# Kernel tuning notes

Hardware: AMD Instinct MI355X
Metric: run time of the kernel (lower is better)

The kernel has to match this reference:

```python
import jax, jax.numpy as jnp
import numpy as np

VOCAB = 32000
EMB = 512
HEADS = 8
HEAD_DIM = EMB // HEADS
MLP = 2048
LAYERS = 6
KERNEL_EPS = 1e-3  # performer generalized-attention kernel_epsilon
LN_EPS = 1e-6


def sinusoidal_pos_emb(seq_len, dim):
    pos = np.arange(seq_len)[:, None].astype(np.float32)
    div = np.exp(np.arange(0, dim, 2).astype(np.float32) * (-np.log(10000.0) / dim))
    pe = np.zeros((seq_len, dim), dtype=np.float32)
    pe[:, 0::2] = np.sin(pos * div)
    pe[:, 1::2] = np.cos(pos * div)
    return jnp.asarray(pe)


def setup_inputs() -> dict:
    key = jax.random.key(0)
    ks = jax.random.split(key, 16)
    B, S = 4, 4096
    s_emb = 1.0 / np.sqrt(EMB)
    s_head = 1.0 / np.sqrt(HEAD_DIM)
    s_mlp = 1.0 / np.sqrt(MLP)
    return {
        'tokens': jax.random.randint(ks[0], (B, S), 0, VOCAB),
        'embed': jax.random.normal(ks[1], (VOCAB, EMB), jnp.float32) * s_emb,
        'Wq': jax.random.normal(ks[2], (LAYERS, EMB, HEADS, HEAD_DIM), jnp.float32) * s_emb,
        'Wk': jax.random.normal(ks[3], (LAYERS, EMB, HEADS, HEAD_DIM), jnp.float32) * s_emb,
        'Wv': jax.random.normal(ks[4], (LAYERS, EMB, HEADS, HEAD_DIM), jnp.float32) * s_emb,
        'Wo': jax.random.normal(ks[5], (LAYERS, HEADS, HEAD_DIM, EMB), jnp.float32) * s_head,
        'ln1_s': jnp.ones((LAYERS, EMB), jnp.float32),
        'ln1_b': jnp.zeros((LAYERS, EMB), jnp.float32),
        'W1': jax.random.normal(ks[6], (LAYERS, EMB, MLP), jnp.float32) * s_emb,
        'b1': jnp.zeros((LAYERS, MLP), jnp.float32),
        'W2': jax.random.normal(ks[7], (LAYERS, MLP, EMB), jnp.float32) * s_mlp,
        'b2': jnp.zeros((LAYERS, EMB), jnp.float32),
        'ln2_s': jnp.ones((LAYERS, EMB), jnp.float32),
        'ln2_b': jnp.zeros((LAYERS, EMB), jnp.float32),
        'lnf_s': jnp.ones((EMB,), jnp.float32),
        'lnf_b': jnp.zeros((EMB,), jnp.float32),
    }


def layer_norm(x, s, b):
    mu = jnp.mean(x, axis=-1, keepdims=True)
    var = jnp.mean(jnp.square(x - mu), axis=-1, keepdims=True)
    return (x - mu) * jax.lax.rsqrt(var + LN_EPS) * s + b


def favor_generalized_attention(x, Wq, Wk, Wv, Wo):
    # Performer generalized attention, deterministic ReLU feature map,
    # renormalized (bidirectional): O(S * m * d) linear attention.
    q = jnp.einsum('bsd,dhf->bshf', x, Wq)
    k = jnp.einsum('bsd,dhf->bshf', x, Wk)
    v = jnp.einsum('bsd,dhf->bshf', x, Wv)
    pq = jax.nn.relu(q) + KERNEL_EPS  # phi(q): [B,S,H,F]
    pk = jax.nn.relu(k) + KERNEL_EPS  # phi(k)
    kv = jnp.einsum('bshf,bshe->bhfe', pk, v)          # [B,H,F,E]
    num = jnp.einsum('bshf,bhfe->bshe', pq, kv)        # numerator
    den = jnp.einsum('bshf,bhf->bsh', pq, pk.sum(axis=1))  # renormalizer
    attn = num / den[..., None]
    return jnp.einsum('bshe,hed->bsd', attn, Wo)


def reference(tokens, embed, Wq, Wk, Wv, Wo, ln1_s, ln1_b, W1, b1, W2, b2,
              ln2_s, ln2_b, lnf_s, lnf_b):
    B, S = tokens.shape
    x = embed[tokens] + sinusoidal_pos_emb(S, EMB)[None, :, :]
    for l in range(LAYERS):
        h = layer_norm(x, ln1_s[l], ln1_b[l])
        x = x + favor_generalized_attention(h, Wq[l], Wk[l], Wv[l], Wo[l])
        h = layer_norm(x, ln2_s[l], ln2_b[l])
        h = jax.nn.gelu(h @ W1[l] + b1[l]) @ W2[l] + b2[l]
        x = x + h
    return layer_norm(x, lnf_s, lnf_b)
```

## Files before the change

### kernel.cpp

```cpp
#include <hip/hip_runtime.h>

typedef float f32x4 __attribute__((ext_vector_type(4)));
typedef __bf16 bf16x8 __attribute__((ext_vector_type(8)));

#define NROWS 16384
#define SEQ   4096
#define EMBD  512
#define MLPD  2048

__device__ inline float gelu_tanh(float x) {
    float t = 0.7978845608028654f * (x + 0.044715f * x * x * x);
    float e = __expf(2.f * t);
    float th = 1.f - 2.f / (1.f + e);
    return 0.5f * x * (1.f + th);
}

#define GLOAD16(gp, lp)                                                        \
    __builtin_amdgcn_global_load_lds(                                          \
        (const __attribute__((address_space(1))) void*)(gp),                   \
        (__attribute__((address_space(3))) void*)(lp), 16, 0, 0)

__global__ void pos_kernel(float* __restrict__ pos) {
    int i = blockIdx.x * 256 + threadIdx.x;
    int s = i >> 8, j = i & 255;
    float div = __expf((float)j * (-2.f * 9.210340371976184f / 512.f));
    float a = (float)s * div;
    pos[(size_t)s * 512 + 2 * j]     = sinf(a);
    pos[(size_t)s * 512 + 2 * j + 1] = cosf(a);
}

__global__ void embed_kernel(const int* __restrict__ tokens,
                             const float* __restrict__ embed,
                             const float* __restrict__ pos,
                             float* __restrict__ x) {
    int row = blockIdx.x;
    int t = threadIdx.x;
    int s = row & (SEQ - 1);
    int tok = tokens[row];
    f32x4 e = *(const f32x4*)(embed + (size_t)tok * 512 + t * 4);
    f32x4 p = *(const f32x4*)(pos + (size_t)s * 512 + t * 4);
    e += p;
    *(f32x4*)(x + (size_t)row * 512 + t * 4) = e;
}

__global__ void transpose_bf16(const float* __restrict__ in, __bf16* __restrict__ out,
                               int K, int N, size_t in_lstride, size_t out_lstride) {
    __shared__ float tile[32][33];
    in  += (size_t)blockIdx.z * in_lstride;
    out += (size_t)blockIdx.z * out_lstride;
    int n0 = blockIdx.x * 32, k0 = blockIdx.y * 32;
    int tx = threadIdx.x, ty = threadIdx.y;
    #pragma unroll
    for (int i = 0; i < 32; i += 8)
        tile[ty + i][tx] = in[(size_t)(k0 + ty + i) * N + n0 + tx];
    __syncthreads();
    #pragma unroll
    for (int i = 0; i < 32; i += 8)
        out[(size_t)(n0 + ty + i) * K + k0 + tx] = (__bf16)tile[tx][ty + i];
}

template<int OUTBF>
__global__ __launch_bounds__(256) void ln_kernel(
    const float* __restrict__ x, const float* __restrict__ gamma,
    const float* __restrict__ beta, __bf16* __restrict__ outb,
    float* __restrict__ outf) {
    int lane = threadIdx.x & 63;
    size_t row = (size_t)blockIdx.x * 4 + (threadIdx.x >> 6);
    const float* xr = x + row * 512 + lane * 8;
    f32x4 v0 = *(const f32x4*)xr;
    f32x4 v1 = *(const f32x4*)(xr + 4);
    float sum = (v0[0] + v0[1]) + (v0[2] + v0[3]) + (v1[0] + v1[1]) + (v1[2] + v1[3]);
    #pragma unroll
    for (int off = 32; off; off >>= 1) sum += __shfl_xor(sum, off);
    float mu = sum * (1.f / 512.f);
    float vs = 0.f;
    #pragma unroll
    for (int j = 0; j < 4; j++) {
        float d0 = v0[j] - mu; vs += d0 * d0;
        float d1 = v1[j] - mu; vs += d1 * d1;
    }
    #pragma unroll
    for (int off = 32; off; off >>= 1) vs += __shfl_xor(vs, off);
    float inv = rsqrtf(vs * (1.f / 512.f) + 1e-6f);
    const float* gp = gamma + lane * 8;
    const float* bp = beta + lane * 8;
    f32x4 g0 = *(const f32x4*)gp, g1 = *(const f32x4*)(gp + 4);
    f32x4 bb0 = *(const f32x4*)bp, bb1 = *(const f32x4*)(bp + 4);
    float o[8];
    #pragma unroll
    for (int j = 0; j < 4; j++) {
        o[j]     = (v0[j] - mu) * inv * g0[j] + bb0[j];
        o[4 + j] = (v1[j] - mu) * inv * g1[j] + bb1[j];
    }
    if (OUTBF) {
        bf16x8 ov;
        #pragma unroll
        for (int j = 0; j < 8; j++) ov[j] = (__bf16)o[j];
        *(bf16x8*)(outb + row * 512 + lane * 8) = ov;
    } else {
        f32x4 o0 = {o[0], o[1], o[2], o[3]};
        f32x4 o1 = {o[4], o[5], o[6], o[7]};
        *(f32x4*)(outf + row * 512 + lane * 8) = o0;
        *(f32x4*)(outf + row * 512 + lane * 8 + 4) = o1;
    }
}

template<int EPI, int K>
__global__ __launch_bounds__(256, 4) void gemm_bt(
    const __bf16* __restrict__ A, const __bf16* __restrict__ BT,
    float* __restrict__ Cf, __bf16* __restrict__ Cb,
    const float* __restrict__ bias, int N, int nbn) {
    constexpr int NT = K / 32;
    __shared__ __align__(16) __bf16 Abuf[2][128 * 32];
    __shared__ __align__(16) __bf16 Bbuf[2][128 * 32];
    const int t = threadIdx.x;
    const int lane = t & 63;
    const int wave = t >> 6;
    const int wr = wave >> 1, wc = wave & 1;
    const int nblk = gridDim.x;
    const int q = nblk >> 3, r = nblk & 7;
    const int xcd = blockIdx.x & 7, loc = blockIdx.x >> 3;
    const int swz = (xcd < r ? xcd * (q + 1) : r * (q + 1) + (xcd - r) * q) + loc;
    const int m0 = (swz / nbn) * 128, n0 = (swz % nbn) * 128;
    const int fr = lane & 15, fc = lane >> 4;

    const __bf16* Aps[2];
    const __bf16* Bps[2];
    int lslot[2];
    #pragma unroll
    for (int j = 0; j < 2; j++) {
        int slot = t + 256 * j;
        int row = slot >> 2, cp = slot & 3;
        int sc = cp ^ ((row >> 1) & 3);
        Aps[j] = A  + (size_t)(m0 + row) * K + sc * 8;
        Bps[j] = BT + (size_t)(n0 + row) * K + sc * 8;
        lslot[j] = slot * 8;
    }

    f32x4 acc[4][4];
    #pragma unroll
    for (int m = 0; m < 4; m++)
        #pragma unroll
        for (int n = 0; n < 4; n++)
            acc[m][n] = (f32x4){0.f, 0.f, 0.f, 0.f};

    auto stage = [&](int koff, __bf16* Ad, __bf16* Bd) {
        #pragma unroll
        for (int j = 0; j < 2; j++) {
            GLOAD16(Aps[j] + koff, Ad + lslot[j]);
            GLOAD16(Bps[j] + koff, Bd + lslot[j]);
        }
    };

    int cur = 0;
    stage(0, Abuf[0], Bbuf[0]);

    for (int s = 0; s < NT; s++) {
        __bf16* Ac = Abuf[cur];     __bf16* Bc = Bbuf[cur];
        if (s + 1 < NT) {
            stage((s + 1) * 32, Abuf[cur ^ 1], Bbuf[cur ^ 1]);
            asm volatile("s_waitcnt vmcnt(4)" ::: "memory");
        } else {
            asm volatile("s_waitcnt vmcnt(0)" ::: "memory");
        }
        __builtin_amdgcn_s_barrier();

        bf16x8 af[4], bfr[4];
        #pragma unroll
        for (int m = 0; m < 4; m++) {
            int ra = wr * 64 + m * 16 + fr;
            int rb = wc * 64 + m * 16 + fr;
            af[m]  = *(const bf16x8*)(Ac + ra * 32 + ((fc ^ ((ra >> 1) & 3)) << 3));
            bfr[m] = *(const bf16x8*)(Bc + rb * 32 + ((fc ^ ((rb >> 1) & 3)) << 3));
        }
        __builtin_amdgcn_s_setprio(1);
        #pragma unroll
        for (int m = 0; m < 4; m++)
            #pragma unroll
            for (int n = 0; n < 4; n++)
                acc[m][n] = __builtin_amdgcn_mfma_f32_16x16x32_bf16(af[m], bfr[n], acc[m][n], 0, 0, 0);
        __builtin_amdgcn_s_setprio(0);
        __builtin_amdgcn_s_barrier();
        cur ^= 1;
    }

    const int cr = (lane >> 4) * 4;
    const int cc = lane & 15;
    #pragma unroll
    for (int m = 0; m < 4; m++) {
        #pragma unroll
        for (int n = 0; n < 4; n++) {
            #pragma unroll
            for (int r2 = 0; r2 < 4; r2++) {
                int grow = m0 + wr * 64 + m * 16 + cr + r2;
                int gcol = n0 + wc * 64 + n * 16 + cc;
                size_t idx = (size_t)grow * N + gcol;
                float val = acc[m][n][r2];
                if (EPI == 1) {
                    if (gcol < 1024) val = fmaxf(val, 0.f) + 1e-3f;
                    Cb[idx] = (__bf16)val;
                } else if (EPI == 2) {
                    Cf[idx] += val;
                } else if (EPI == 3) {
                    val += bias[gcol];
                    Cb[idx] = (__bf16)gelu_tanh(val);
                } else if (EPI == 4) {
                    Cf[idx] += val + bias[gcol];
                } else {
                    Cf[idx] = val;
                }
            }
        }
    }
}

__global__ __launch_bounds__(256) void kv_partial(const __bf16* __restrict__ qkvb,
                                                  float* __restrict__ part) {
    int bh = blockIdx.x;
    int chunk = blockIdx.y;
    int b = bh >> 3, hh = bh & 7;
    int t = threadIdx.x;
    int f = t & 63, eg = t >> 6;
    size_t base = ((size_t)b * SEQ + (size_t)chunk * 64) * 1536;
    const __bf16* kcol = qkvb + base + 512 + hh * 64 + f;
    const __bf16* vrow = qkvb + base + 1024 + hh * 64 + eg * 16;
    float psum = 0.f;
    f32x4 a0 = {0.f,0.f,0.f,0.f}, a1 = a0, a2 = a0, a3 = a0;
    for (int s = 0; s < 64; s++) {
        size_t o = (size_t)s * 1536;
        float pk = (float)kcol[o];
        psum += pk;
        bf16x8 w0 = *(const bf16x8*)(vrow + o);
        bf16x8 w1 = *(const bf16x8*)(vrow + o + 8);
        #pragma unroll
        for (int j = 0; j < 4; j++) {
            a0[j] += (float)w0[j]     * pk;
            a1[j] += (float)w0[4 + j] * pk;
            a2[j] += (float)w1[j]     * pk;
            a3[j] += (float)w1[4 + j] * pk;
        }
    }
    float* dst = part + ((size_t)chunk * 32 + bh) * 4160 + (size_t)f * 65 + eg * 16;
    #pragma unroll
    for (int j = 0; j < 4; j++) { dst[j] = a0[j]; dst[4+j] = a1[j]; dst[8+j] = a2[j]; dst[12+j] = a3[j]; }
    if (eg == 0) dst[64] = psum;
}

__global__ void kv_reduce(const float* __restrict__ part, float* __restrict__ kvfin) {
    int i = blockIdx.x * 256 + threadIdx.x;
    if (i >= 32 * 4160) return;
    float s = 0.f;
    #pragma unroll 8
    for (int c = 0; c < 64; c++) s += part[(size_t)c * (32 * 4160) + i];
    kvfin[i] = s;
}

__global__ __launch_bounds__(256) void num_attn(const __bf16* __restrict__ qkvb,
                                                const float* __restrict__ kvfin,
                                                __bf16* __restrict__ attn) {
    __shared__ float kvs[64][68];
    __shared__ float ps[64];
    int bh = blockIdx.x, chunk = blockIdx.y;
    int b = bh >> 3, hh = bh & 7;
    const float* src = kvfin + (size_t)bh * 4160;
    for (int i = threadIdx.x; i < 4160; i += 256) {
        int f = i / 65, e = i - f * 65;
        if (e < 64) kvs[f][e] = src[i]; else ps[f] = src[i];
    }
    __syncthreads();
    int t = threadIdx.x;
    int r = t >> 1, e0 = (t & 1) * 32;
    size_t row = (size_t)b * SEQ + (size_t)chunk * 128 + r;
    const __bf16* pqr = qkvb + row * 1536 + hh * 64;
    float pq[64];
    #pragma unroll
    for (int j = 0; j < 8; j++) {
        bf16x8 v = *(const bf16x8*)(pqr + 8 * j);
        #pragma unroll
        for (int k = 0; k < 8; k++) pq[8 * j + k] = (float)v[k];
    }
    float den = 0.f;
    #pragma unroll
    for (int f = 0; f < 64; f++) den += pq[f] * ps[f];
    f32x4 acc[8];
    #pragma unroll
    for (int j = 0; j < 8; j++) acc[j] = (f32x4){0.f,0.f,0.f,0.f};
    for (int f = 0; f < 64; f++) {
        float p = pq[f];
        #pragma unroll
        for (int j = 0; j < 8; j++) acc[j] += *(const f32x4*)(&kvs[f][e0 + 4 * j]) * p;
    }
    float rd = 1.f / den;
    __bf16* op = attn + row * 512 + hh * 64 + e0;
    #pragma unroll
    for (int j2 = 0; j2 < 4; j2++) {
        bf16x8 ov;
        #pragma unroll
        for (int k = 0; k < 8; k++) ov[k] = (__bf16)(acc[j2 * 2 + k / 4][k % 4] * rd);
        *(bf16x8*)(op + j2 * 8) = ov;
    }
}

extern "C" void kernel_launch(void* const* d_in, const int* in_sizes, int n_in,
                              void* d_out, int out_size, void* d_ws, size_t ws_size,
                              hipStream_t stream) {
    const int*   tokens = (const int*)d_in[0];
    const float* embed  = (const float*)d_in[1];
    const float* Wq     = (const float*)d_in[2];
    const float* Wk     = (const float*)d_in[3];
    const float* Wv     = (const float*)d_in[4];
    const float* Wo     = (const float*)d_in[5];
    const float* ln1_s  = (const float*)d_in[6];
    const float* ln1_b  = (const float*)d_in[7];
    const float* W1     = (const float*)d_in[8];
    const float* b1     = (const float*)d_in[9];
    const float* W2     = (const float*)d_in[10];
    const float* b2     = (const float*)d_in[11];
    const float* ln2_s  = (const float*)d_in[12];
    const float* ln2_b  = (const float*)d_in[13];
    const float* lnf_s  = (const float*)d_in[14];
    const float* lnf_b  = (const float*)d_in[15];
    float* out = (float*)d_out;

    float* ws = (float*)d_ws;
    size_t off = 0;
    float* pos = ws;               off += 2097152;
    float* x   = ws + off;         off += 8388608;
    __bf16* h    = (__bf16*)(ws + off); off += 4194304;
    __bf16* attn = (__bf16*)(ws + off); off += 4194304;
    __bf16* qkvb = (__bf16*)(ws + off);
    __bf16* hid  = (__bf16*)(ws + off); off += 16777216;
    float* kvpart = ws + off;      off += 64 * 32 * 4160;
    float* kvfin  = ws + off;      off += 32 * 4160;
    __bf16* wbuf  = (__bf16*)(ws + off);

    pos_kernel<<<4096, 256, 0, stream>>>(pos);
    transpose_bf16<<<dim3(16, 16, 6), dim3(32, 8), 0, stream>>>(Wq, wbuf,          512, 512,  262144, 3145728);
    transpose_bf16<<<dim3(16, 16, 6), dim3(32, 8), 0, stream>>>(Wk, wbuf + 262144, 512, 512,  262144, 3145728);
    transpose_bf16<<<dim3(16, 16, 6), dim3(32, 8), 0, stream>>>(Wv, wbuf + 524288, 512, 512,  262144, 3145728);
    transpose_bf16<<<dim3(16, 16, 6), dim3(32, 8), 0, stream>>>(Wo, wbuf + 786432, 512, 512,  262144, 3145728);
    transpose_bf16<<<dim3(64, 16, 6), dim3(32, 8), 0, stream>>>(W1, wbuf + 1048576, 512, 2048, 1048576, 3145728);
    transpose_bf16<<<dim3(16, 64, 6), dim3(32, 8), 0, stream>>>(W2, wbuf + 2097152, 2048, 512, 1048576, 3145728);
    embed_kernel<<<16384, 128, 0, stream>>>(tokens, embed, pos, x);

    for (int l = 0; l < 6; l++) {
        const __bf16* wl = wbuf + (size_t)l * 3145728;
        ln_kernel<1><<<4096, 256, 0, stream>>>(x, ln1_s + l * 512, ln1_b + l * 512, h, nullptr);
        gemm_bt<1, 512><<<1536, 256, 0, stream>>>(h, wl, nullptr, qkvb, nullptr, 1536, 12);
        kv_partial<<<dim3(32, 64), 256, 0, stream>>>(qkvb, kvpart);
        kv_reduce<<<520, 256, 0, stream>>>(kvpart, kvfin);
        num_attn<<<dim3(32, 32), 256, 0, stream>>>(qkvb, kvfin, attn);
        gemm_bt<2, 512><<<512, 256, 0, stream>>>(attn, wl + 786432, x, nullptr, nullptr, 512, 4);
        ln_kernel<1><<<4096, 256, 0, stream>>>(x, ln2_s + l * 512, ln2_b + l * 512, h, nullptr);
        gemm_bt<3, 512><<<2048, 256, 0, stream>>>(h, wl + 1048576, nullptr, hid, b1 + (size_t)l * 2048, 2048, 16);
        gemm_bt<4, 2048><<<512, 256, 0, stream>>>(hid, wl + 2097152, x, nullptr, b2 + (size_t)l * 512, 512, 4);
    }
    ln_kernel<0><<<4096, 256, 0, stream>>>(x, lnf_s, lnf_b, nullptr, out);
}
```

Before: 1.763 ms.

## Triple-buffer GEMM LDS pipeline and use 64-row tiles for N=512 GEMMs

The GEMM now uses a three-stage LDS ring buffer, so loads for tile s+2 are issued while tile s is computed, with vmcnt waits adjusted to match. A BM template parameter lets the two N=512 GEMMs (attention output projection and MLP down-projection) use 64x128 tiles with four waves split along N. This doubles their grid from 512 to 1024 blocks, giving better CU occupancy on a 256-CU part. The cost is more LDS per block and lower arithmetic intensity per block for the smaller tiles, since each B tile is reused across fewer rows.

```diff
diff --git a/kernel.cpp b/kernel.cpp
--- a/kernel.cpp
+++ b/kernel.cpp
@@ -105,83 +105,102 @@
     }
 }
 
-template<int EPI, int K>
+template<int EPI, int K, int BM>
 __global__ __launch_bounds__(256, 4) void gemm_bt(
     const __bf16* __restrict__ A, const __bf16* __restrict__ BT,
     float* __restrict__ Cf, __bf16* __restrict__ Cb,
     const float* __restrict__ bias, int N, int nbn) {
     constexpr int NT = K / 32;
-    __shared__ __align__(16) __bf16 Abuf[2][128 * 32];
-    __shared__ __align__(16) __bf16 Bbuf[2][128 * 32];
+    constexpr int AL = BM / 64;
+    constexpr int NREP = (BM == 128) ? 4 : 2;
+    __shared__ __align__(16) __bf16 Asm[3][BM * 32];
+    __shared__ __align__(16) __bf16 Bsm[3][128 * 32];
     const int t = threadIdx.x;
     const int lane = t & 63;
     const int wave = t >> 6;
-    const int wr = wave >> 1, wc = wave & 1;
+    const int wr = (BM == 128) ? (wave >> 1) : 0;
+    const int wc = (BM == 128) ? (wave & 1) : wave;
     const int nblk = gridDim.x;
     const int q = nblk >> 3, r = nblk & 7;
     const int xcd = blockIdx.x & 7, loc = blockIdx.x >> 3;
     const int swz = (xcd < r ? xcd * (q + 1) : r * (q + 1) + (xcd - r) * q) + loc;
-    const int m0 = (swz / nbn) * 128, n0 = (swz % nbn) * 128;
+    const int m0 = (swz / nbn) * BM, n0 = (swz % nbn) * 128;
     const int fr = lane & 15, fc = lane >> 4;
 
-    const __bf16* Aps[2];
+    const __bf16* Aps[AL];
     const __bf16* Bps[2];
-    int lslot[2];
+    int aslot[AL], bslot[2];
+    #pragma unroll
+    for (int j = 0; j < AL; j++) {
+        int slot = t + 256 * j;
+        int row = slot >> 2, cp = slot & 3;
+        int sc = cp ^ ((row >> 1) & 3);
+        Aps[j] = A + (size_t)(m0 + row) * K + sc * 8;
+        aslot[j] = slot * 8;
+    }
     #pragma unroll
     for (int j = 0; j < 2; j++) {
         int slot = t + 256 * j;
         int row = slot >> 2, cp = slot & 3;
         int sc = cp ^ ((row >> 1) & 3);
-        Aps[j] = A  + (size_t)(m0 + row) * K + sc * 8;
         Bps[j] = BT + (size_t)(n0 + row) * K + sc * 8;
-        lslot[j] = slot * 8;
-    }
-
-    f32x4 acc[4][4];
+        bslot[j] = slot * 8;
+    }
+
+    f32x4 acc[4][NREP];
     #pragma unroll
     for (int m = 0; m < 4; m++)
         #pragma unroll
-        for (int n = 0; n < 4; n++)
+        for (int n = 0; n < NREP; n++)
             acc[m][n] = (f32x4){0.f, 0.f, 0.f, 0.f};
 
     auto stage = [&](int koff, __bf16* Ad, __bf16* Bd) {
         #pragma unroll
-        for (int j = 0; j < 2; j++) {
-            GLOAD16(Aps[j] + koff, Ad + lslot[j]);
-            GLOAD16(Bps[j] + koff, Bd + lslot[j]);
-        }
+        for (int j = 0; j < AL; j++) GLOAD16(Aps[j] + koff, Ad + aslot[j]);
+        #pragma unroll
+        for (int j = 0; j < 2; j++) GLOAD16(Bps[j] + koff, Bd + bslot[j]);
     };
 
-    int cur = 0;
-    stage(0, Abuf[0], Bbuf[0]);
+    __bf16 *A0 = Asm[0], *A1 = Asm[1], *A2 = Asm[2];
+    __bf16 *B0 = Bsm[0], *B1 = Bsm[1], *B2 = Bsm[2];
+    stage(0, A0, B0);
+    stage(32, A1, B1);
 
     for (int s = 0; s < NT; s++) {
-        __bf16* Ac = Abuf[cur];     __bf16* Bc = Bbuf[cur];
-        if (s + 1 < NT) {
-            stage((s + 1) * 32, Abuf[cur ^ 1], Bbuf[cur ^ 1]);
-            asm volatile("s_waitcnt vmcnt(4)" ::: "memory");
+        if (s + 2 < NT) {
+            stage((s + 2) * 32, A2, B2);
+            if constexpr (BM == 128) asm volatile("s_waitcnt vmcnt(8)" ::: "memory");
+            else                     asm volatile("s_waitcnt vmcnt(6)" ::: "memory");
+        } else if (s + 1 < NT) {
+            if constexpr (BM == 128) asm volatile("s_waitcnt vmcnt(4)" ::: "memory");
+            else                     asm volatile("s_waitcnt vmcnt(3)" ::: "memory");
         } else {
             asm volatile("s_waitcnt vmcnt(0)" ::: "memory");
         }
         __builtin_amdgcn_s_barrier();
 
-        bf16x8 af[4], bfr[4];
+        bf16x8 af[4], bfr[NREP];
         #pragma unroll
         for (int m = 0; m < 4; m++) {
             int ra = wr * 64 + m * 16 + fr;
-            int rb = wc * 64 + m * 16 + fr;
-            af[m]  = *(const bf16x8*)(Ac + ra * 32 + ((fc ^ ((ra >> 1) & 3)) << 3));
-            bfr[m] = *(const bf16x8*)(Bc + rb * 32 + ((fc ^ ((rb >> 1) & 3)) << 3));
+            af[m] = *(const bf16x8*)(A0 + ra * 32 + ((fc ^ ((ra >> 1) & 3)) << 3));
+        }
+        #pragma unroll
+        for (int n = 0; n < NREP; n++) {
+            int rb = wc * (16 * NREP) + n * 16 + fr;
+            bfr[n] = *(const bf16x8*)(B0 + rb * 32 + ((fc ^ ((rb >> 1) & 3)) << 3));
         }
         __builtin_amdgcn_s_setprio(1);
         #pragma unroll
         for (int m = 0; m < 4; m++)
             #pragma unroll
-            for (int n = 0; n < 4; n++)
+            for (int n = 0; n < NREP; n++)
                 acc[m][n] = __builtin_amdgcn_mfma_f32_16x16x32_bf16(af[m], bfr[n], acc[m][n], 0, 0, 0);
         __builtin_amdgcn_s_setprio(0);
         __builtin_amdgcn_s_barrier();
-        cur ^= 1;
+
+        __bf16* ta = A0; A0 = A1; A1 = A2; A2 = ta;
+        __bf16* tb = B0; B0 = B1; B1 = B2; B2 = tb;
     }
 
     const int cr = (lane >> 4) * 4;
@@ -189,11 +208,11 @@
     #pragma unroll
     for (int m = 0; m < 4; m++) {
         #pragma unroll
-        for (int n = 0; n < 4; n++) {
+        for (int n = 0; n < NREP; n++) {
             #pragma unroll
             for (int r2 = 0; r2 < 4; r2++) {
                 int grow = m0 + wr * 64 + m * 16 + cr + r2;
-                int gcol = n0 + wc * 64 + n * 16 + cc;
+                int gcol = n0 + wc * (16 * NREP) + n * 16 + cc;
                 size_t idx = (size_t)grow * N + gcol;
                 float val = acc[m][n][r2];
                 if (EPI == 1) {
@@ -346,14 +365,14 @@
     for (int l = 0; l < 6; l++) {
         const __bf16* wl = wbuf + (size_t)l * 3145728;
         ln_kernel<1><<<4096, 256, 0, stream>>>(x, ln1_s + l * 512, ln1_b + l * 512, h, nullptr);
-        gemm_bt<1, 512><<<1536, 256, 0, stream>>>(h, wl, nullptr, qkvb, nullptr, 1536, 12);
+        gemm_bt<1, 512, 128><<<1536, 256, 0, stream>>>(h, wl, nullptr, qkvb, nullptr, 1536, 12);
         kv_partial<<<dim3(32, 64), 256, 0, stream>>>(qkvb, kvpart);
         kv_reduce<<<520, 256, 0, stream>>>(kvpart, kvfin);
         num_attn<<<dim3(32, 32), 256, 0, stream>>>(qkvb, kvfin, attn);
-        gemm_bt<2, 512><<<512, 256, 0, stream>>>(attn, wl + 786432, x, nullptr, nullptr, 512, 4);
+        gemm_bt<2, 512, 64><<<1024, 256, 0, stream>>>(attn, wl + 786432, x, nullptr, nullptr, 512, 4);
         ln_kernel<1><<<4096, 256, 0, stream>>>(x, ln2_s + l * 512, ln2_b + l * 512, h, nullptr);
-        gemm_bt<3, 512><<<2048, 256, 0, stream>>>(h, wl + 1048576, nullptr, hid, b1 + (size_t)l * 2048, 2048, 16);
-        gemm_bt<4, 2048><<<512, 256, 0, stream>>>(hid, wl + 2097152, x, nullptr, b2 + (size_t)l * 512, 512, 4);
+        gemm_bt<3, 512, 128><<<2048, 256, 0, stream>>>(h, wl + 1048576, nullptr, hid, b1 + (size_t)l * 2048, 2048, 16);
+        gemm_bt<4, 2048, 64><<<1024, 256, 0, stream>>>(hid, wl + 2097152, x, nullptr, b2 + (size_t)l * 512, 512, 4);
     }
     ln_kernel<0><<<4096, 256, 0, stream>>>(x, lnf_s, lnf_b, nullptr, out);
 }
```

After: 1.761 ms. Within noise of the previous version (-0.1%).

## Enlarge GEMM tile to 256x128 with 8 waves and interleaved ping-pong pipeline

Applied to the files above, without the earlier changes.

The bf16 GEMM now uses 512-thread blocks computing 256x128 tiles with a BK=64 step split into two 32-wide halves. Global-to-LDS prefetch of the next tile is spread across four MFMA phases, with barriers and setprio around each phase, so memory traffic overlaps with compute. Launch grids are halved to match. The aim is better operand reuse and latency hiding. In exchange there are more barriers per step, twice the LDS per block, and fewer blocks per CU.

```diff
diff --git a/kernel.cpp b/kernel.cpp
--- a/kernel.cpp
+++ b/kernel.cpp
@@ -106,36 +106,61 @@
 }
 
 template<int EPI, int K>
-__global__ __launch_bounds__(256, 4) void gemm_bt(
+__global__ __launch_bounds__(512, 2) void gemm_bt(
     const __bf16* __restrict__ A, const __bf16* __restrict__ BT,
     float* __restrict__ Cf, __bf16* __restrict__ Cb,
     const float* __restrict__ bias, int N, int nbn) {
-    constexpr int NT = K / 32;
-    __shared__ __align__(16) __bf16 Abuf[2][128 * 32];
-    __shared__ __align__(16) __bf16 Bbuf[2][128 * 32];
+    constexpr int NK = K / 64;
+    __shared__ __align__(16) __bf16 Ab[2][2][256 * 32];
+    __shared__ __align__(16) __bf16 Bb[2][2][128 * 32];
     const int t = threadIdx.x;
     const int lane = t & 63;
     const int wave = t >> 6;
-    const int wr = wave >> 1, wc = wave & 1;
+    const int wr = wave >> 1;
+    const int wc = wave & 1;
     const int nblk = gridDim.x;
     const int q = nblk >> 3, r = nblk & 7;
     const int xcd = blockIdx.x & 7, loc = blockIdx.x >> 3;
     const int swz = (xcd < r ? xcd * (q + 1) : r * (q + 1) + (xcd - r) * q) + loc;
-    const int m0 = (swz / nbn) * 128, n0 = (swz % nbn) * 128;
+    const int m0 = (swz / nbn) * 256, n0 = (swz % nbn) * 128;
     const int fr = lane & 15, fc = lane >> 4;
 
-    const __bf16* Aps[2];
-    const __bf16* Bps[2];
-    int lslot[2];
-    #pragma unroll
-    for (int j = 0; j < 2; j++) {
-        int slot = t + 256 * j;
+    const __bf16* gA[2];
+    int lA[2];
+    #pragma unroll
+    for (int jj = 0; jj < 2; jj++) {
+        int slot = t + 512 * jj;
         int row = slot >> 2, cp = slot & 3;
         int sc = cp ^ ((row >> 1) & 3);
-        Aps[j] = A  + (size_t)(m0 + row) * K + sc * 8;
-        Bps[j] = BT + (size_t)(n0 + row) * K + sc * 8;
-        lslot[j] = slot * 8;
-    }
+        gA[jj] = A + (size_t)(m0 + row) * K + sc * 8;
+        lA[jj] = slot * 8;
+    }
+    const __bf16* gB;
+    int lB;
+    {
+        int row = t >> 2, cp = t & 3;
+        int sc = cp ^ ((row >> 1) & 3);
+        gB = BT + (size_t)(n0 + row) * K + sc * 8;
+        lB = t * 8;
+    }
+
+    auto stageA = [&](int kt, int half, int buf) {
+        int koff = kt * 64 + half * 32;
+        GLOAD16(gA[0] + koff, &Ab[buf][half][lA[0]]);
+        GLOAD16(gA[1] + koff, &Ab[buf][half][lA[1]]);
+    };
+    auto stageB = [&](int kt, int half, int buf) {
+        int koff = kt * 64 + half * 32;
+        GLOAD16(gB + koff, &Bb[buf][half][lB]);
+    };
+    auto rdA = [&](int buf, int kk, int mi) -> bf16x8 {
+        int row = wr * 64 + mi * 16 + fr;
+        return *(const bf16x8*)&Ab[buf][kk][row * 32 + ((fc ^ ((row >> 1) & 3)) << 3)];
+    };
+    auto rdB = [&](int buf, int kk, int n) -> bf16x8 {
+        int row = wc * 64 + n * 16 + fr;
+        return *(const bf16x8*)&Bb[buf][kk][row * 32 + ((fc ^ ((row >> 1) & 3)) << 3)];
+    };
 
     f32x4 acc[4][4];
     #pragma unroll
@@ -144,44 +169,74 @@
         for (int n = 0; n < 4; n++)
             acc[m][n] = (f32x4){0.f, 0.f, 0.f, 0.f};
 
-    auto stage = [&](int koff, __bf16* Ad, __bf16* Bd) {
-        #pragma unroll
-        for (int j = 0; j < 2; j++) {
-            GLOAD16(Aps[j] + koff, Ad + lslot[j]);
-            GLOAD16(Bps[j] + koff, Bd + lslot[j]);
-        }
-    };
-
-    int cur = 0;
-    stage(0, Abuf[0], Bbuf[0]);
-
-    for (int s = 0; s < NT; s++) {
-        __bf16* Ac = Abuf[cur];     __bf16* Bc = Bbuf[cur];
-        if (s + 1 < NT) {
-            stage((s + 1) * 32, Abuf[cur ^ 1], Bbuf[cur ^ 1]);
-            asm volatile("s_waitcnt vmcnt(4)" ::: "memory");
+    stageA(0, 0, 0); stageB(0, 0, 0); stageA(0, 1, 0); stageB(0, 1, 0);
+    asm volatile("s_waitcnt vmcnt(3)" ::: "memory");
+    __builtin_amdgcn_s_barrier();
+
+    for (int j = 0; j < NK; ++j) {
+        const int cur = j & 1, nxt = cur ^ 1;
+        const bool pf = (j + 1 < NK);
+        bf16x8 bfr[4], af0, af1;
+        #pragma unroll
+        for (int n = 0; n < 4; n++) bfr[n] = rdB(cur, 0, n);
+        af0 = rdA(cur, 0, 0); af1 = rdA(cur, 0, 1);
+        if (pf) stageA(j + 1, 0, nxt);
+        __builtin_amdgcn_s_barrier();
+        asm volatile("s_waitcnt lgkmcnt(0)" ::: "memory");
+        __builtin_amdgcn_s_setprio(1);
+        #pragma unroll
+        for (int n = 0; n < 4; n++) {
+            acc[0][n] = __builtin_amdgcn_mfma_f32_16x16x32_bf16(af0, bfr[n], acc[0][n], 0, 0, 0);
+            acc[1][n] = __builtin_amdgcn_mfma_f32_16x16x32_bf16(af1, bfr[n], acc[1][n], 0, 0, 0);
+        }
+        __builtin_amdgcn_s_setprio(0);
+        __builtin_amdgcn_s_barrier();
+        af0 = rdA(cur, 0, 2); af1 = rdA(cur, 0, 3);
+        if (pf) {
+            stageB(j + 1, 0, nxt);
+            asm volatile("s_waitcnt vmcnt(3)" ::: "memory");
         } else {
             asm volatile("s_waitcnt vmcnt(0)" ::: "memory");
         }
         __builtin_amdgcn_s_barrier();
-
-        bf16x8 af[4], bfr[4];
-        #pragma unroll
-        for (int m = 0; m < 4; m++) {
-            int ra = wr * 64 + m * 16 + fr;
-            int rb = wc * 64 + m * 16 + fr;
-            af[m]  = *(const bf16x8*)(Ac + ra * 32 + ((fc ^ ((ra >> 1) & 3)) << 3));
-            bfr[m] = *(const bf16x8*)(Bc + rb * 32 + ((fc ^ ((rb >> 1) & 3)) << 3));
-        }
+        asm volatile("s_waitcnt lgkmcnt(0)" ::: "memory");
         __builtin_amdgcn_s_setprio(1);
         #pragma unroll
-        for (int m = 0; m < 4; m++)
-            #pragma unroll
-            for (int n = 0; n < 4; n++)
-                acc[m][n] = __builtin_amdgcn_mfma_f32_16x16x32_bf16(af[m], bfr[n], acc[m][n], 0, 0, 0);
+        for (int n = 0; n < 4; n++) {
+            acc[2][n] = __builtin_amdgcn_mfma_f32_16x16x32_bf16(af0, bfr[n], acc[2][n], 0, 0, 0);
+            acc[3][n] = __builtin_amdgcn_mfma_f32_16x16x32_bf16(af1, bfr[n], acc[3][n], 0, 0, 0);
+        }
         __builtin_amdgcn_s_setprio(0);
         __builtin_amdgcn_s_barrier();
-        cur ^= 1;
+        #pragma unroll
+        for (int n = 0; n < 4; n++) bfr[n] = rdB(cur, 1, n);
+        af0 = rdA(cur, 1, 0); af1 = rdA(cur, 1, 1);
+        if (pf) stageA(j + 1, 1, nxt);
+        __builtin_amdgcn_s_barrier();
+        asm volatile("s_waitcnt lgkmcnt(0)" ::: "memory");
+        __builtin_amdgcn_s_setprio(1);
+        #pragma unroll
+        for (int n = 0; n < 4; n++) {
+            acc[0][n] = __builtin_amdgcn_mfma_f32_16x16x32_bf16(af0, bfr[n], acc[0][n], 0, 0, 0);
+            acc[1][n] = __builtin_amdgcn_mfma_f32_16x16x32_bf16(af1, bfr[n], acc[1][n], 0, 0, 0);
+        }
+        __builtin_amdgcn_s_setprio(0);
+        __builtin_amdgcn_s_barrier();
+        af0 = rdA(cur, 1, 2); af1 = rdA(cur, 1, 3);
+        if (pf) {
+            stageB(j + 1, 1, nxt);
+            asm volatile("s_waitcnt vmcnt(3)" ::: "memory");
+        }
+        __builtin_amdgcn_s_barrier();
+        asm volatile("s_waitcnt lgkmcnt(0)" ::: "memory");
+        __builtin_amdgcn_s_setprio(1);
+        #pragma unroll
+        for (int n = 0; n < 4; n++) {
+            acc[2][n] = __builtin_amdgcn_mfma_f32_16x16x32_bf16(af0, bfr[n], acc[2][n], 0, 0, 0);
+            acc[3][n] = __builtin_amdgcn_mfma_f32_16x16x32_bf16(af1, bfr[n], acc[3][n], 0, 0, 0);
+        }
+        __builtin_amdgcn_s_setprio(0);
+        __builtin_amdgcn_s_barrier();
     }
 
     const int cr = (lane >> 4) * 4;
@@ -346,14 +401,14 @@
     for (int l = 0; l < 6; l++) {
         const __bf16* wl = wbuf + (size_t)l * 3145728;
         ln_kernel<1><<<4096, 256, 0, stream>>>(x, ln1_s + l * 512, ln1_b + l * 512, h, nullptr);
-        gemm_bt<1, 512><<<1536, 256, 0, stream>>>(h, wl, nullptr, qkvb, nullptr, 1536, 12);
+        gemm_bt<1, 512><<<768, 512, 0, stream>>>(h, wl, nullptr, qkvb, nullptr, 1536, 12);
         kv_partial<<<dim3(32, 64), 256, 0, stream>>>(qkvb, kvpart);
         kv_reduce<<<520, 256, 0, stream>>>(kvpart, kvfin);
         num_attn<<<dim3(32, 32), 256, 0, stream>>>(qkvb, kvfin, attn);
-        gemm_bt<2, 512><<<512, 256, 0, stream>>>(attn, wl + 786432, x, nullptr, nullptr, 512, 4);
+        gemm_bt<2, 512><<<256, 512, 0, stream>>>(attn, wl + 786432, x, nullptr, nullptr, 512, 4);
         ln_kernel<1><<<4096, 256, 0, stream>>>(x, ln2_s + l * 512, ln2_b + l * 512, h, nullptr);
-        gemm_bt<3, 512><<<2048, 256, 0, stream>>>(h, wl + 1048576, nullptr, hid, b1 + (size_t)l * 2048, 2048, 16);
-        gemm_bt<4, 2048><<<512, 256, 0, stream>>>(hid, wl + 2097152, x, nullptr, b2 + (size_t)l * 512, 512, 4);
+        gemm_bt<3, 512><<<1024, 512, 0, stream>>>(h, wl + 1048576, nullptr, hid, b1 + (size_t)l * 2048, 2048, 16);
+        gemm_bt<4, 2048><<<256, 512, 0, stream>>>(hid, wl + 2097152, x, nullptr, b2 + (size_t)l * 512, 512, 4);
     }
     ln_kernel<0><<<4096, 256, 0, stream>>>(x, lnf_s, lnf_b, nullptr, out);
 }
```

Result: slower. 1.889 ms (+7.1%).
